# Kernel optimization log

Hardware: AMD Instinct MI355X
Metric: run time of the kernel (lower is better)

## Reference

```python
import jax, jax.numpy as jnp
import numpy as np

H_HEADS = 16
DECAY_C = 0.7408182206817179  # math.exp(-0.3)


def _gelu(x):
    return jax.nn.gelu(x, approximate=False)  # torch nn.GELU default = exact erf


def _mlp(x, W1, b1, W2, b2):
    return _gelu(x @ W1 + b1) @ W2 + b2


def setup_inputs():
    B, T, C = 4, 2048, 1024
    L = max(64, C // 8)      # lora_dim = 128
    E = int(C * 1.2)         # expanded_dim = 1228
    key = jax.random.key(0)
    ctr = [0]
    def rn(shape, s=0.02):
        ctr[0] += 1
        return jax.random.normal(jax.random.fold_in(key, ctr[0]), shape, jnp.float32) * s
    z = lambda *s: jnp.zeros(s, jnp.float32)
    inp = {
        "queries": rn((B, T, C), 1.0),
        "keys": rn((B, T, C), 1.0),
        "values": rn((B, T, C), 1.0),
        "attn_mask": jnp.ones((B, T), dtype=bool),
        "mu_r": rn((C,)), "mu_k": rn((C,)), "mu_v": rn((C,)),
        "mu_g": rn((C,)), "mu_a": rn((C,)), "mu_d": rn((C,)),
        "dA": rn((C, L)), "dB": rn((L, C)), "db": z(C),
        "aA": rn((C, L)), "aB": rn((L, C)), "ab": z(C),
        "gA": rn((C, L)), "gB": rn((L, C)),
        "rW1": rn((C, E)), "rb1": z(E), "rW2": rn((E, C)), "rb2": z(C),
        "kW1": rn((C, E)), "kb1": z(E), "kW2": rn((E, C)), "kb2": z(C),
        "vW1": rn((C, E)), "vb1": z(E), "vW2": rn((E, C)), "vb2": z(C),
        "oW1": rn((C, E)), "ob1": z(E), "oW2": rn((E, C)), "ob2": z(C),
        "rem_mult": rn((C,), 0.05),
        "iclr_mix": jnp.full((C,), 0.7, jnp.float32),
        "bonus_mult": jnp.full((C,), 1.2, jnp.float32),
        "ln_g": jnp.ones((C,), jnp.float32), "ln_b": z(C),
    }
    return inp


def _forward(queries, mu_r, mu_k, mu_v, mu_g, mu_a, mu_d,
             dA, dB, db, aA, aB, ab, gA, gB,
             rW1, rb1, rW2, rb2, kW1, kb1, kW2, kb2,
             vW1, vb1, vW2, vb2, oW1, ob1, oW2, ob2,
             rem_mult, iclr_mix, bonus_mult, ln_g, ln_b):
    B, T, C = queries.shape
    H = H_HEADS
    N = C // H
    r = _mlp(queries + mu_r, rW1, rb1, rW2, rb2)
    k = _mlp(queries + mu_k, kW1, kb1, kW2, kb2)
    v = _mlp(queries + mu_v, vW1, vb1, vW2, vb2)
    gate = jax.nn.sigmoid(((queries + mu_g) @ gA) @ gB)
    iclr = jax.nn.sigmoid(((queries + mu_a) @ aA) @ ab + ((queries + mu_a) @ aA) @ aB) if False else jax.nn.sigmoid(((queries + mu_a) @ aA) @ aB + ab)
    decay = jnp.exp(-DECAY_C * jax.nn.sigmoid(jnp.tanh(((queries + mu_d) @ dA) @ dB + db)))
    removal_k = k * rem_mult
    replacement_k = k * (1.0 + (iclr - 1.0) * iclr_mix)  # lerp(ones, iclr, mix)
    rh = r.reshape(B, T, H, N)
    rkh = replacement_k.reshape(B, T, H, N)
    vh = v.reshape(B, T, H, N)
    dh = decay.reshape(B, T, H, N)
    ah = iclr.reshape(B, T, H, N)
    rmh = removal_k.reshape(B, T, H, N)
    kn = rmh / jnp.maximum(jnp.linalg.norm(rmh, axis=-1, keepdims=True), 1e-12)  # F.normalize
    # Sequential matrix-state recurrence. G_t = diag(d) - kn (a*kn)^T, so
    # G_t @ S = d[:,None]*S - kn[:,None] * ((a*kn) @ S)  -- rank-1, O(N^2)/step.
    xs = tuple(jnp.swapaxes(a, 0, 1) for a in (dh, ah, kn, rkh, vh, rh))  # [T,B,H,N]
    def step(wkv, x):
        d, a, knt, rk, vt, rt = x
        tmp = jnp.einsum('bhj,bhjk->bhk', a * knt, wkv)
        wkv = d[..., None] * wkv - knt[..., None] * tmp[:, :, None, :] \
              + vt[..., None] * rk[:, :, None, :]
        return wkv, jnp.einsum('bhij,bhj->bhi', wkv, rt)
    wkv0 = jnp.zeros((B, H, N, N), queries.dtype)
    _, out_t = jax.lax.scan(step, wkv0, xs)
    out = jnp.swapaxes(out_t, 0, 1)  # [B,T,H,N]
    bonus = (jnp.sum(rh * rkh, -1, keepdims=True) * 0.2) * vh * bonus_mult.reshape(1, 1, H, N)
    out = (out + bonus).reshape(B, T, C)
    mu = jnp.mean(out, -1, keepdims=True)
    var = jnp.mean((out - mu) ** 2, -1, keepdims=True)
    out = (out - mu) / jnp.sqrt(var + 1e-6) * ln_g + ln_b  # ln_x, eps=1e-6
    out = out * gate
    out = _mlp(out, oW1, ob1, oW2, ob2)  # W_output; dropout is identity in eval
    return out


def reference(queries, keys, values, attn_mask,
              mu_r, mu_k, mu_v, mu_g, mu_a, mu_d,
              dA, dB, db, aA, aB, ab, gA, gB,
              rW1, rb1, rW2, rb2, kW1, kb1, kW2, kb2,
              vW1, vb1, vW2, vb2, oW1, ob1, oW2, ob2,
              rem_mult, iclr_mix, bonus_mult, ln_g, ln_b):
    del keys, values, attn_mask  # accepted but unused by the module's forward
    return _forward(queries, mu_r, mu_k, mu_v, mu_g, mu_a, mu_d,
                    dA, dB, db, aA, aB, ab, gA, gB,
                    rW1, rb1, rW2, rb2, kW1, kb1, kW2, kb2,
                    vW1, vb1, vW2, vb2, oW1, ob1, oW2, ob2,
                    rem_mult, iclr_mix, bonus_mult, ln_g, ln_b)
```

## Files before the change

### kernel.cpp

```cpp
#include <hip/hip_runtime.h>
#include <hip/hip_bf16.h>
#include <math.h>


#define BB 4
#define TT 2048
#define CC 1024
#define HH 16
#define NN 64
#define LL 128
#define EE 1228
#define EPAD 1280
#define MM (BB*TT)
#define TCH 32
#define NSEG 4
#define WARMCH 2
#define DECAY_C_F 0.7408182206817179f

typedef __attribute__((ext_vector_type(8))) short s16x8;
typedef __attribute__((ext_vector_type(4))) float f32x4;

#define GLOAD_LDS16(gp, lp) \
    __builtin_amdgcn_global_load_lds((const __attribute__((address_space(1))) void*)(gp), \
                                     (__attribute__((address_space(3))) void*)(lp), 16, 0, 0)

__global__ __launch_bounds__(256) void fold_pass1_z(
    const float* __restrict__ mu0, const float* __restrict__ mu1, const float* __restrict__ mu2,
    const float* __restrict__ W0,  const float* __restrict__ W1_, const float* __restrict__ W2_,
    float* __restrict__ partial, int ldW, int E, int ldP, int pslice) {
    const float* mu = blockIdx.z == 0 ? mu0 : (blockIdx.z == 1 ? mu1 : mu2);
    const float* W  = blockIdx.z == 0 ? W0  : (blockIdx.z == 1 ? W1_ : W2_);
    partial += (size_t)blockIdx.z * pslice;
    const int l = threadIdx.x & 63;
    const int e = blockIdx.x * 64 + l;
    const int pg = threadIdx.x >> 6;
    const int c0 = blockIdx.y * 64;
    float s = 0.f;
    if (e < E)
        for (int c = c0 + pg; c < c0 + 64; c += 4) s += mu[c] * W[(size_t)c * ldW + e];
    __shared__ float red[4][64];
    red[pg][l] = s;
    __syncthreads();
    if (pg == 0 && e < E)
        partial[(size_t)blockIdx.y * ldP + e] = red[0][l] + red[1][l] + red[2][l] + red[3][l];
}

__global__ void fold_pass2_z(const float* __restrict__ partial,
                             const float* b0, const float* b1, const float* b2,
                             float* __restrict__ outv,
                             int P, int ldP, int pslice, int E, int Epad, int oslice) {
    const float* bias = blockIdx.z == 0 ? b0 : (blockIdx.z == 1 ? b1 : b2);
    partial += (size_t)blockIdx.z * pslice;
    outv    += (size_t)blockIdx.z * oslice;
    int e = blockIdx.x * blockDim.x + threadIdx.x;
    if (e >= Epad) return;
    float s = 0.f;
    if (e < E) {
        s = bias ? bias[e] : 0.f;
        for (int p = 0; p < P; ++p) s += partial[(size_t)p * ldP + e];
    }
    outv[e] = s;
}

__global__ void cast_f32_bf16(const float* __restrict__ in, __hip_bfloat16* __restrict__ out, int n4) {
    int i = blockIdx.x * blockDim.x + threadIdx.x;
    if (i >= n4) return;
    float4 v = ((const float4*)in)[i];
    __hip_bfloat16 o[4] = {__float2bfloat16(v.x), __float2bfloat16(v.y),
                           __float2bfloat16(v.z), __float2bfloat16(v.w)};
    *(ulong1*)&out[i * 4] = *(ulong1*)o;
}

__global__ void transpose_cast_z(const float* s0, const float* s1, const float* s2,
                                 __hip_bfloat16* __restrict__ outT, size_t dslice,
                                 int Rin, int Cin, int Rpad, int Cpad) {
    const float* in = blockIdx.z == 0 ? s0 : (blockIdx.z == 1 ? s1 : s2);
    outT += (size_t)blockIdx.z * dslice;
    __shared__ float t[32][33];
    const int r0 = blockIdx.x * 32, c0 = blockIdx.y * 32;
    const int tx = threadIdx.x, ty = threadIdx.y;
    #pragma unroll
    for (int j = 0; j < 4; ++j) {
        int r = r0 + ty + j * 8, c = c0 + tx;
        t[ty + j * 8][tx] = (r < Rin && c < Cin) ? in[(size_t)r * Cin + c] : 0.f;
    }
    __syncthreads();
    #pragma unroll
    for (int j = 0; j < 4; ++j) {
        int c = c0 + ty + j * 8, r = r0 + tx;
        if (c < Cpad && r < Rpad) outT[(size_t)c * Rpad + r] = __float2bfloat16(t[tx][ty + j * 8]);
    }
}

template<int ACT, int OBF, int PADZ>
__global__ __launch_bounds__(256) void gemm_mfma(const __hip_bfloat16* __restrict__ A,
                                                 const __hip_bfloat16* __restrict__ Bt,
                                                 const float* __restrict__ bias,
                                                 void* __restrict__ Cptr,
                                                 int M, int N, int K,
                                                 int ldA, int ldB, int ldC,
                                                 size_t zA, size_t zB, size_t zBias, size_t zC) {
    __shared__ __hip_bfloat16 As[128 * 32];
    __shared__ __hip_bfloat16 Bs[128 * 32];
    const int tid = threadIdx.x;
    const int wid = tid >> 6, lane = tid & 63;
    const int wm = wid >> 1, wn = wid & 1;
    const int bm = blockIdx.y * 128, bn = blockIdx.x * 128;
    A  += (size_t)blockIdx.z * zA;
    Bt += (size_t)blockIdx.z * zB;
    if (bias) bias += (size_t)blockIdx.z * zBias;
    const size_t zc = (size_t)blockIdx.z * zC;

    const __hip_bfloat16* srcA[2];
    const __hip_bfloat16* srcB[2];
    #pragma unroll
    for (int i = 0; i < 2; ++i) {
        int off = (wid * 2 + i) * 1024 + lane * 16;
        int r = off >> 6;
        int c = (off >> 4) & 3;
        int cs = c ^ ((r >> 1) & 3);
        srcA[i] = A  + (size_t)(bm + r) * ldA + cs * 8;
        srcB[i] = Bt + (size_t)(bn + r) * ldB + cs * 8;
    }

    f32x4 acc[4][4];
    #pragma unroll
    for (int i = 0; i < 4; ++i)
        #pragma unroll
        for (int j = 0; j < 4; ++j) acc[i][j] = (f32x4){0.f, 0.f, 0.f, 0.f};

    for (int k0 = 0; k0 < K; k0 += 32) {
        #pragma unroll
        for (int i = 0; i < 2; ++i) {
            GLOAD_LDS16(srcA[i] + k0, (char*)As + (wid * 2 + i) * 1024);
            GLOAD_LDS16(srcB[i] + k0, (char*)Bs + (wid * 2 + i) * 1024);
        }
        __syncthreads();
        s16x8 af[4], bfr[4];
        #pragma unroll
        for (int mi = 0; mi < 4; ++mi) {
            int r = wm * 64 + mi * 16 + (lane & 15);
            int c = (lane >> 4) ^ ((r >> 1) & 3);
            af[mi] = *(const s16x8*)((const char*)As + r * 64 + c * 16);
        }
        #pragma unroll
        for (int ni = 0; ni < 4; ++ni) {
            int r = wn * 64 + ni * 16 + (lane & 15);
            int c = (lane >> 4) ^ ((r >> 1) & 3);
            bfr[ni] = *(const s16x8*)((const char*)Bs + r * 64 + c * 16);
        }
        #pragma unroll
        for (int mi = 0; mi < 4; ++mi)
            #pragma unroll
            for (int ni = 0; ni < 4; ++ni)
                acc[mi][ni] = __builtin_amdgcn_mfma_f32_16x16x32_bf16(af[mi], bfr[ni], acc[mi][ni], 0, 0, 0);
        __syncthreads();
    }

    #pragma unroll
    for (int ni = 0; ni < 4; ++ni) {
        const int col = bn + wn * 64 + ni * 16 + (lane & 15);
        const bool valid = (col < N);
        const float bc = (valid && bias) ? bias[col] : 0.f;
        #pragma unroll
        for (int mi = 0; mi < 4; ++mi) {
            #pragma unroll
            for (int reg = 0; reg < 4; ++reg) {
                const int row = bm + wm * 64 + mi * 16 + (lane >> 4) * 4 + reg;
                float y = 0.f;
                if (valid) {
                    float x = acc[mi][ni][reg] + bc;
                    if (ACT == 1)      y = 0.5f * x * (1.0f + erff(x * 0.7071067811865475f));
                    else if (ACT == 2) y = 1.0f / (1.0f + expf(-x));
                    else if (ACT == 3) { float sg = 1.0f / (1.0f + expf(-tanhf(x))); y = expf(-DECAY_C_F * sg); }
                    else               y = x;
                }
                if (valid || PADZ) {
                    if (OBF) ((__hip_bfloat16*)Cptr)[zc + (size_t)row * ldC + col] = __float2bfloat16(y);
                    else     ((float*)Cptr)[zc + (size_t)row * ldC + col] = y;
                }
            }
        }
    }
}

#define P_T0(i,j)   pool[0     + (i)*68 + (j)]
#define P_WT(i,j)   pool[4352  + (i)*68 + (j)]
#define P_KP(i,j)   pool[6528  + (i)*68 + (j)]
#define P_P2t(i,j)  pool[6528  + (i)*36 + (j)]
#define P_NU(i,j)   pool[8704  + (i)*68 + (j)]
#define P_GRt(i,j)  pool[8704  + (i)*36 + (j)]
#define P_RKM(i,j)  pool[10880 + (i)*68 + (j)]
#define P_RRM(i,j)  pool[13056 + (i)*68 + (j)]
#define P_GM(i,j)   pool[15232 + (i)*68 + (j)]
#define P_KPT(i,j)  pool[19712 + (i)*36 + (j)]
#define P_NUT(i,j)  pool[22016 + (i)*36 + (j)]
#define P_DCT(i,j)  pool[26624 + (i)*36 + (j)]
#define P_AT(i,j)   pool[28928 + (i)*36 + (j)]
#define P_BM(i,j)   pool[30080 + (i)*36 + (j)]
#define P_SEG(i,j)  pool[31232 + (i)*64 + (j)]
#define LD4(expr)   (*(const float4*)&(expr))
#define FMA4(acc, s, v) { (acc).x = fmaf((s), (v).x, (acc).x); (acc).y = fmaf((s), (v).y, (acc).y); \
                          (acc).z = fmaf((s), (v).z, (acc).z); (acc).w = fmaf((s), (v).w, (acc).w); }

__global__ __launch_bounds__(512) void recurrence_chunked(
    const float* __restrict__ kbuf, const __hip_bfloat16* __restrict__ iclr,
    const __hip_bfloat16* __restrict__ dbuf, const float* __restrict__ vbuf,
    const float* __restrict__ rbuf,
    const float* __restrict__ rem_mult, const float* __restrict__ iclr_mix,
    const float* __restrict__ bonus_mult, float* __restrict__ outb) {
    __shared__ float pool[31488];
    const int bh = blockIdx.x & 63, seg = blockIdx.x >> 6;
    const int b = bh >> 4, h = bh & 15;
    const int tid = threadIdx.x, lane = tid & 63, wid = tid >> 6;
    const size_t gbase = ((size_t)b * TT) * CC + (size_t)h * NN;

    for (int i = tid; i < 4352; i += 512) pool[i] = 0.f;
    const int c0 = tid & 63;
    const float remc = rem_mult[h * NN + c0];
    const float mixc = iclr_mix[h * NN + c0];
    __syncthreads();

    const int cout0 = (seg == 0) ? 0 : (seg == 1) ? 18 : (seg == 2) ? 34 : 49;
    const int lenq  = (seg == 0) ? 18 : (seg == 1) ? 16 : 15;
    const int ce    = cout0 + lenq;
    const int cb    = (seg == 0) ? 0 : cout0 - WARMCH;

    for (int chk = cb; chk < ce; ++chk) {
        const bool emit = (chk >= cout0);
        const int tg0 = chk * TCH;
        #pragma unroll
        for (int i = 0; i < 4; ++i) {
            int idx = tid + 512 * i;
            int t = idx >> 6, c = idx & 63;
            size_t off = gbase + (size_t)(tg0 + t) * CC + c;
            float kx = kbuf[off];
            float ax = __bfloat162float(iclr[off]);
            float rk = kx * (1.f + (ax - 1.f) * mixc);
            P_WT(t, c) = ax;
            P_KP(t, c) = kx * remc;
            P_RKM(t, c) = rk;
            P_NU(t, c) = vbuf[off];
            if (emit) P_RRM(t, c) = rbuf[off];
            P_DCT(c, t) = __bfloat162float(dbuf[off]);
        }
        __syncthreads();
        #pragma unroll
        for (int rr = 0; rr < 4; ++rr) {
            int t = wid + rr * 8;
            float v = P_KP(t, lane);
            float ss = v * v;
            #pragma unroll
            for (int s = 32; s; s >>= 1) ss += __shfl_xor(ss, s);
            float kn = v / fmaxf(sqrtf(ss), 1e-12f);
            P_KP(t, lane) = kn;
            P_WT(t, lane) = P_WT(t, lane) * kn;
        }
        float lc[8];
        const int ccs = tid & 63, sgm = tid >> 6, t0s = (sgm & 3) * 8;
        if (tid < 256) {
            float pp_ = 1.f;
            #pragma unroll
            for (int j = 0; j < 8; ++j) { pp_ *= P_DCT(ccs, t0s + j); lc[j] = pp_; }
            P_SEG(sgm, ccs) = pp_;
        }
        __syncthreads();
        if (tid < 256) {
            float m = 1.f;
            for (int s = 0; s < sgm; ++s) m *= P_SEG(s, ccs);
            float dcprev = m;
            #pragma unroll
            for (int j = 0; j < 8; ++j) {
                int t = t0s + j;
                float dcur = m * lc[j];
                P_WT(t, ccs) *= dcprev;
                float inv = 1.f / dcur;
                float kap = P_KP(t, ccs) * inv; P_KP(t, ccs) = kap; P_KPT(ccs, t) = kap;
                float nu  = P_NU(t, ccs) * inv; P_NU(t, ccs) = nu;  P_NUT(ccs, t) = nu;
                P_DCT(ccs, t) = dcur;
                dcprev = dcur;
            }
        }
        __syncthreads();
        #pragma unroll
        for (int u = 0; u < 2; ++u) {
            const int at = wid * 2 + u;
            const int s = (at >> 2) * 8 + (lane >> 3), t = (at & 3) * 8 + (lane & 7);
            float acc = 0.f;
            #pragma unroll
            for (int kc = 0; kc < 16; ++kc) {
                float4 a = LD4(P_KP(s, kc * 4));
                float4 bb = LD4(P_WT(t, kc * 4));
                acc += a.x * bb.x + a.y * bb.y + a.z * bb.z + a.w * bb.w;
            }
            P_AT(s, t) = (s < t) ? acc : 0.f;
        }
        #pragma unroll
        for (int u = 0; u < 2; ++u) {
            const int bt = wid * 2 + u;
            const int t = (bt >> 2) * 8 + (lane >> 3), s = (bt & 3) * 8 + (lane & 7);
            float acc = 0.f;
            #pragma unroll
            for (int kc = 0; kc < 16; ++kc) {
                float4 a = LD4(P_WT(t, kc * 4));
                float4 bb = LD4(P_NU(s, kc * 4));
                acc += a.x * bb.x + a.y * bb.y + a.z * bb.z + a.w * bb.w;
            }
            P_BM(t, s) = (s < t) ? acc : 0.f;
        }
        {
            const int t = wid * 4 + (lane >> 4);
            const int q4 = (lane & 15) * 4;
            float4 acc = {0.f, 0.f, 0.f, 0.f};
            #pragma unroll
            for (int j4 = 0; j4 < 16; ++j4) {
                float4 w4 = LD4(P_WT(t, j4 * 4));
                float4 ta = LD4(P_T0(j4 * 4 + 0, q4));
                float4 tb = LD4(P_T0(j4 * 4 + 1, q4));
                float4 tc = LD4(P_T0(j4 * 4 + 2, q4));
                float4 td = LD4(P_T0(j4 * 4 + 3, q4));
                FMA4(acc, w4.x, ta); FMA4(acc, w4.y, tb);
                FMA4(acc, w4.z, tc); FMA4(acc, w4.w, td);
            }
            *(float4*)&P_GM(t, q4) = acc;
        }
        __syncthreads();
        {
            const int t = wid * 4 + (lane >> 4);
            const int q4 = (lane & 15) * 4;
            float4 acc = {0.f, 0.f, 0.f, 0.f};
            #pragma unroll
            for (int s4 = 0; s4 < 8; ++s4) {
                float4 bm4 = LD4(P_BM(t, s4 * 4));
                float4 ra = LD4(P_RKM(s4 * 4 + 0, q4));
                float4 rb = LD4(P_RKM(s4 * 4 + 1, q4));
                float4 rc = LD4(P_RKM(s4 * 4 + 2, q4));
                float4 rd = LD4(P_RKM(s4 * 4 + 3, q4));
                FMA4(acc, bm4.x, ra); FMA4(acc, bm4.y, rb);
                FMA4(acc, bm4.z, rc); FMA4(acc, bm4.w, rd);
            }
            float4 g = LD4(P_GM(t, q4));
            g.x += acc.x; g.y += acc.y; g.z += acc.z; g.w += acc.w;
            *(float4*)&P_GM(t, q4) = g;
        }
        __syncthreads();
        if (wid == 0) {
            float g[32];
            #pragma unroll
            for (int t = 0; t < 32; ++t) g[t] = P_GM(t, lane);
            #pragma unroll
            for (int s = 0; s < 31; ++s) {
                #pragma unroll
                for (int t = s + 1; t < 32; ++t) g[t] -= P_AT(s, t) * g[s];
            }
            #pragma unroll
            for (int t = 0; t < 32; ++t) P_GM(t, lane) = g[t];
        } else if (emit) {
            for (int tile = wid - 1; tile < 16; tile += 7) {
                int t = (tile >> 2) * 8 + (lane >> 3), s = (tile & 3) * 8 + (lane & 7);
                float acc = 0.f;
                #pragma unroll
                for (int kc = 0; kc < 16; ++kc) {
                    float4 a = LD4(P_RRM(t, kc * 4));
                    float4 bb = LD4(P_RKM(s, kc * 4));
                    acc += a.x * bb.x + a.y * bb.y + a.z * bb.z + a.w * bb.w;
                }
                P_P2t(t, s) = (s <= t) ? acc : 0.f;
            }
        }
        __syncthreads();
        if (emit) {
            for (int tile = wid; tile < 16; tile += 8) {
                int t = (tile >> 2) * 8 + (lane >> 3), s = (tile & 3) * 8 + (lane & 7);
                float acc = 0.f;
                #pragma unroll
                for (int kc = 0; kc < 16; ++kc) {
                    float4 a = LD4(P_RRM(t, kc * 4));
                    float4 bb = LD4(P_GM(s, kc * 4));
                    acc += a.x * bb.x + a.y * bb.y + a.z * bb.z + a.w * bb.w;
                }
                P_GRt(t, s) = (s <= t) ? acc : 0.f;
            }
            __syncthreads();
            for (int tile = wid; tile < 32; tile += 8) {
                int i = (tile >> 2) * 8 + (lane >> 3), t = (tile & 3) * 8 + (lane & 7);
                float a1 = 0.f, a2 = 0.f, a3 = 0.f;
                #pragma unroll
                for (int j4 = 0; j4 < 16; ++j4) {
                    float4 a = LD4(P_T0(i, j4 * 4));
                    float4 bb = LD4(P_RRM(t, j4 * 4));
                    a1 += a.x * bb.x + a.y * bb.y + a.z * bb.z + a.w * bb.w;
                }
                #pragma unroll
                for (int s4 = 0; s4 < 8; ++s4) {
                    float4 a = LD4(P_NUT(i, s4 * 4));
                    float4 bb = LD4(P_P2t(t, s4 * 4));
                    a2 += a.x * bb.x + a.y * bb.y + a.z * bb.z + a.w * bb.w;
                    float4 c = LD4(P_KPT(i, s4 * 4));
                    float4 d = LD4(P_GRt(t, s4 * 4));
                    a3 += c.x * d.x + c.y * d.y + c.z * d.z + c.w * d.w;
                }
                float diag = 0.2f * bonus_mult[h * NN + i] * P_NUT(i, t) * P_P2t(t, t);
                outb[gbase + (size_t)(tg0 + t) * CC + i] = P_DCT(i, t) * (a1 + a2 + diag - a3);
            }
            __syncthreads();
        }
        #pragma unroll
        for (int u = 0; u < 2; ++u) {
            const int m = wid * 2 + u;
            const int pr = (m & 7) * 8 + (lane >> 3);
            const int q4 = (m >> 3) * 32 + (lane & 7) * 4;
            float4 a1 = {0.f, 0.f, 0.f, 0.f}, a2 = {0.f, 0.f, 0.f, 0.f};
            #pragma unroll
            for (int s = 0; s < 32; ++s) {
                const float kp = P_KPT(pr, s);
                const float nu = P_NUT(pr, s);
                float4 g4 = LD4(P_GM(s, q4));
                float4 rk4 = LD4(P_RKM(s, q4));
                FMA4(a1, kp, g4);
                FMA4(a2, nu, rk4);
            }
            const float dc = P_DCT(pr, 31);
            float4 t0 = LD4(P_T0(pr, q4));
            t0.x = dc * (t0.x - a1.x + a2.x);
            t0.y = dc * (t0.y - a1.y + a2.y);
            t0.z = dc * (t0.z - a1.z + a2.z);
            t0.w = dc * (t0.w - a1.w + a2.w);
            *(float4*)&P_T0(pr, q4) = t0;
        }
        __syncthreads();
    }
}

__global__ __launch_bounds__(256) void ln_gate_kernel(const float* __restrict__ x,
                                                      const __hip_bfloat16* __restrict__ gate,
                                                      const float* __restrict__ g,
                                                      const float* __restrict__ bv,
                                                      __hip_bfloat16* __restrict__ y) {
    const int row = blockIdx.x;
    const float* xr = x + (size_t)row * CC;
    float v[4];
    float s = 0.f;
    #pragma unroll
    for (int j = 0; j < 4; ++j) { v[j] = xr[threadIdx.x + 256 * j]; s += v[j]; }
    __shared__ float red[4], red2[4];
    #pragma unroll
    for (int o = 32; o; o >>= 1) s += __shfl_xor(s, o);
    if ((threadIdx.x & 63) == 0) red[threadIdx.x >> 6] = s;
    __syncthreads();
    const float mean = (red[0] + red[1] + red[2] + red[3]) * (1.f / CC);
    float vs = 0.f;
    #pragma unroll
    for (int j = 0; j < 4; ++j) { float d = v[j] - mean; vs += d * d; }
    #pragma unroll
    for (int o = 32; o; o >>= 1) vs += __shfl_xor(vs, o);
    if ((threadIdx.x & 63) == 0) red2[threadIdx.x >> 6] = vs;
    __syncthreads();
    const float var = (red2[0] + red2[1] + red2[2] + red2[3]) * (1.f / CC);
    const float rstd = rsqrtf(var + 1e-6f);
    #pragma unroll
    for (int j = 0; j < 4; ++j) {
        const int cc = threadIdx.x + 256 * j;
        float o_ = (v[j] - mean) * rstd * g[cc] + bv[cc];
        float gt = __bfloat162float(gate[(size_t)row * CC + cc]);
        y[(size_t)row * CC + cc] = __float2bfloat16(o_ * gt);
    }
}

extern "C" void kernel_launch(void* const* d_in, const int* in_sizes, int n_in,
                              void* d_out, int out_size, void* d_ws, size_t ws_size,
                              hipStream_t stream) {
    const float* q        = (const float*)d_in[0];
    const float* mu_r     = (const float*)d_in[4];
    const float* mu_k     = (const float*)d_in[5];
    const float* mu_v     = (const float*)d_in[6];
    const float* mu_g     = (const float*)d_in[7];
    const float* mu_a     = (const float*)d_in[8];
    const float* mu_d     = (const float*)d_in[9];
    const float* dA       = (const float*)d_in[10];
    const float* dB       = (const float*)d_in[11];
    const float* db       = (const float*)d_in[12];
    const float* aA       = (const float*)d_in[13];
    const float* aB       = (const float*)d_in[14];
    const float* ab       = (const float*)d_in[15];
    const float* gA       = (const float*)d_in[16];
    const float* gB       = (const float*)d_in[17];
    const float* rW1      = (const float*)d_in[18];
    const float* rb1      = (const float*)d_in[19];
    const float* rW2      = (const float*)d_in[20];
    const float* rb2      = (const float*)d_in[21];
    const float* kW1      = (const float*)d_in[22];
    const float* kb1      = (const float*)d_in[23];
    const float* kW2      = (const float*)d_in[24];
    const float* kb2      = (const float*)d_in[25];
    const float* vW1      = (const float*)d_in[26];
    const float* vb1      = (const float*)d_in[27];
    const float* vW2      = (const float*)d_in[28];
    const float* vb2      = (const float*)d_in[29];
    const float* oW1      = (const float*)d_in[30];
    const float* ob1      = (const float*)d_in[31];
    const float* oW2      = (const float*)d_in[32];
    const float* ob2      = (const float*)d_in[33];
    const float* rem_mult = (const float*)d_in[34];
    const float* iclr_mix = (const float*)d_in[35];
    const float* bonus_mult = (const float*)d_in[36];
    const float* ln_g     = (const float*)d_in[37];
    const float* ln_b     = (const float*)d_in[38];
    float* out = (float*)d_out;

    char* p = (char*)d_ws;
    auto alloc = [&](size_t bytes) { char* r = p; p += (bytes + 255) & ~(size_t)255; return r; };
    float* fb_all  = (float*)alloc((size_t)3 * EPAD * 4);
    float* c2_all  = (float*)alloc((size_t)3 * CC * 4);
    float* lt_all  = (float*)alloc((size_t)3 * LL * 4);
    float* cb2_all = (float*)alloc((size_t)3 * CC * 4);
    __hip_bfloat16* qb      = (__hip_bfloat16*)alloc((size_t)MM * CC * 2);
    __hip_bfloat16* W1T_all = (__hip_bfloat16*)alloc((size_t)3 * EPAD * CC * 2);
    __hip_bfloat16* W2T_all = (__hip_bfloat16*)alloc((size_t)3 * CC * EPAD * 2);
    __hip_bfloat16* Hb      = (__hip_bfloat16*)alloc((size_t)MM * 2 * EPAD * 2);
    float*          rkv     = (float*)alloc((size_t)3 * MM * CC * 4);
    __hip_bfloat16* abuf    = (__hip_bfloat16*)alloc((size_t)MM * CC * 2);
    __hip_bfloat16* dbuf    = (__hip_bfloat16*)alloc((size_t)MM * CC * 2);
    __hip_bfloat16* gbuf    = (__hip_bfloat16*)alloc((size_t)MM * CC * 2);
    float* rbuf = rkv;
    float* kbuf = rkv + (size_t)MM * CC;
    float* vbuf = rkv + (size_t)2 * MM * CC;
    float*          pp      = rkv;
    __hip_bfloat16* AT_all  = (__hip_bfloat16*)((char*)rkv + (1 << 18));
    __hip_bfloat16* BT_all  = (__hip_bfloat16*)((char*)rkv + (1 << 18) + 786432);
    __hip_bfloat16* oW1T    = (__hip_bfloat16*)rkv;
    __hip_bfloat16* oW2T    = (__hip_bfloat16*)((char*)rkv + 4194304);
    __hip_bfloat16* tgad    = Hb;

    const dim3 blk(256);
    const dim3 tblk(32, 8);

    hipMemcpyAsync(cb2_all,          rb2, CC * 4, hipMemcpyDeviceToDevice, stream);
    hipMemcpyAsync(cb2_all + CC,     kb2, CC * 4, hipMemcpyDeviceToDevice, stream);
    hipMemcpyAsync(cb2_all + 2 * CC, vb2, CC * 4, hipMemcpyDeviceToDevice, stream);

    fold_pass1_z<<<dim3(20, 16, 3), blk, 0, stream>>>(mu_r, mu_k, mu_v, rW1, kW1, vW1,
                                                      pp, EE, EE, EPAD, 16 * EPAD);
    fold_pass2_z<<<dim3(5, 1, 3), blk, 0, stream>>>(pp, rb1, kb1, vb1, fb_all,
                                                    16, EPAD, 16 * EPAD, EE, EPAD, EPAD);
    fold_pass1_z<<<dim3(2, 16, 3), blk, 0, stream>>>(mu_g, mu_a, mu_d, gA, aA, dA,
                                                     pp, LL, LL, EPAD, 16 * EPAD);
    fold_pass2_z<<<dim3(1, 1, 3), dim3(128), 0, stream>>>(pp, nullptr, nullptr, nullptr, lt_all,
                                                          16, EPAD, 16 * EPAD, LL, LL, LL);
    fold_pass1_z<<<dim3(16, 2, 3), blk, 0, stream>>>(lt_all, lt_all + LL, lt_all + 2 * LL, gB, aB, dB,
                                                     pp, CC, CC, EPAD, 16 * EPAD);
    fold_pass2_z<<<dim3(4, 1, 3), blk, 0, stream>>>(pp, nullptr, ab, db, c2_all,
                                                    2, EPAD, 16 * EPAD, CC, CC, CC);

    transpose_cast_z<<<dim3(32, 40, 3), tblk, 0, stream>>>(rW1, kW1, vW1, W1T_all,
                                                           (size_t)EPAD * CC, CC, EE, CC, EPAD);
    transpose_cast_z<<<dim3(40, 32, 3), tblk, 0, stream>>>(rW2, kW2, vW2, W2T_all,
                                                           (size_t)CC * EPAD, EE, CC, EPAD, CC);
    transpose_cast_z<<<dim3(32, 4, 3), tblk, 0, stream>>>(gA, aA, dA, AT_all,
                                                          (size_t)LL * CC, CC, LL, CC, LL);
    transpose_cast_z<<<dim3(4, 32, 3), tblk, 0, stream>>>(gB, aB, dB, BT_all,
                                                          (size_t)CC * LL, LL, CC, LL, CC);

    cast_f32_bf16<<<dim3(MM * CC / 4 / 256), blk, 0, stream>>>(q, qb, MM * CC / 4);

    gemm_mfma<0,1,0><<<dim3(3, 64, 1), blk, 0, stream>>>(qb, AT_all, nullptr, tgad,
                                                         MM, 384, CC, CC, CC, 384, 0, 0, 0, 0);
    gemm_mfma<2,1,0><<<dim3(8, 64, 1), blk, 0, stream>>>(tgad,       BT_all,               c2_all,          gbuf,
                                                         MM, CC, LL, 384, LL, CC, 0, 0, 0, 0);
    gemm_mfma<2,1,0><<<dim3(8, 64, 1), blk, 0, stream>>>(tgad + LL,  BT_all + (size_t)CC * LL,  c2_all + CC,     abuf,
                                                         MM, CC, LL, 384, LL, CC, 0, 0, 0, 0);
    gemm_mfma<3,1,0><<<dim3(8, 64, 1), blk, 0, stream>>>(tgad + 2 * LL, BT_all + (size_t)2 * CC * LL, c2_all + 2 * CC, dbuf,
                                                         MM, CC, LL, 384, LL, CC, 0, 0, 0, 0);

    gemm_mfma<1,1,0><<<dim3(20, 64, 1), blk, 0, stream>>>(qb, W1T_all, fb_all, Hb,
                                                          MM, 2 * EPAD, CC, CC, CC, 2 * EPAD, 0, 0, 0, 0);
    gemm_mfma<0,0,0><<<dim3(8, 64, 2), blk, 0, stream>>>(Hb, W2T_all, cb2_all, rkv,
                                                         MM, CC, EPAD, 2 * EPAD, EPAD, CC,
                                                         EPAD, (size_t)CC * EPAD, CC, (size_t)MM * CC);
    gemm_mfma<1,1,0><<<dim3(10, 64, 1), blk, 0, stream>>>(qb, W1T_all + (size_t)2 * EPAD * CC, fb_all + 2 * EPAD, Hb,
                                                          MM, EPAD, CC, CC, CC, EPAD, 0, 0, 0, 0);
    gemm_mfma<0,0,0><<<dim3(8, 64, 1), blk, 0, stream>>>(Hb, W2T_all + (size_t)2 * CC * EPAD, cb2_all + 2 * CC, vbuf,
                                                         MM, CC, EPAD, EPAD, EPAD, CC, 0, 0, 0, 0);

    recurrence_chunked<<<dim3(BB * HH * NSEG), dim3(512), 0, stream>>>(
        kbuf, abuf, dbuf, vbuf, rbuf, rem_mult, iclr_mix, bonus_mult, out);

    transpose_cast_z<<<dim3(32, 40, 1), tblk, 0, stream>>>(oW1, oW1, oW1, oW1T,
                                                           0, CC, EE, CC, EPAD);
    transpose_cast_z<<<dim3(40, 32, 1), tblk, 0, stream>>>(oW2, oW2, oW2, oW2T,
                                                           0, EE, CC, EPAD, CC);

    ln_gate_kernel<<<dim3(MM), blk, 0, stream>>>(out, gbuf, ln_g, ln_b, qb);

    gemm_mfma<1,1,1><<<dim3(10, 64, 1), blk, 0, stream>>>(qb, oW1T, ob1, Hb,
                                                          MM, EE, CC, CC, CC, EPAD, 0, 0, 0, 0);
    gemm_mfma<0,0,0><<<dim3(8, 64, 1), blk, 0, stream>>>(Hb, oW2T, ob2, out,
                                                         MM, CC, EPAD, EPAD, EPAD, CC, 0, 0, 0, 0);
}
```

Before: 939.7 us.

## Double GEMM K-tile to 64 and batch r/k/v and LoRA GEMMs

The MFMA GEMM now stages a 64-wide K slice per iteration with an 8-way XOR swizzle, which halves the number of barrier pairs per K loop. The three r/k/v first-layer GEMMs are merged into one wide launch and the second-layer GEMMs into one z-batched launch. The three LoRA up-projections (gate, iclr, decay) also run as one z-batched launch, with the activation chosen per z slice. Shared memory per block doubles, which may lower occupancy, and the hidden buffer grows to hold all three expansions.

```diff
diff --git a/kernel.cpp b/kernel.cpp
--- a/kernel.cpp
+++ b/kernel.cpp
@@ -92,7 +92,7 @@
     }
 }
 
-template<int ACT, int OBF, int PADZ>
+template<int ACT, int ACTZ2, int OBF, int PADZ>
 __global__ __launch_bounds__(256) void gemm_mfma(const __hip_bfloat16* __restrict__ A,
                                                  const __hip_bfloat16* __restrict__ Bt,
                                                  const float* __restrict__ bias,
@@ -100,8 +100,8 @@
                                                  int M, int N, int K,
                                                  int ldA, int ldB, int ldC,
                                                  size_t zA, size_t zB, size_t zBias, size_t zC) {
-    __shared__ __hip_bfloat16 As[128 * 32];
-    __shared__ __hip_bfloat16 Bs[128 * 32];
+    __shared__ __hip_bfloat16 As[128 * 64];
+    __shared__ __hip_bfloat16 Bs[128 * 64];
     const int tid = threadIdx.x;
     const int wid = tid >> 6, lane = tid & 63;
     const int wm = wid >> 1, wn = wid & 1;
@@ -110,15 +110,16 @@
     Bt += (size_t)blockIdx.z * zB;
     if (bias) bias += (size_t)blockIdx.z * zBias;
     const size_t zc = (size_t)blockIdx.z * zC;
-
-    const __hip_bfloat16* srcA[2];
-    const __hip_bfloat16* srcB[2];
-    #pragma unroll
-    for (int i = 0; i < 2; ++i) {
-        int off = (wid * 2 + i) * 1024 + lane * 16;
-        int r = off >> 6;
-        int c = (off >> 4) & 3;
-        int cs = c ^ ((r >> 1) & 3);
+    const int act = (ACTZ2 >= 0 && blockIdx.z == 2) ? ACTZ2 : ACT;
+
+    const __hip_bfloat16* srcA[4];
+    const __hip_bfloat16* srcB[4];
+    #pragma unroll
+    for (int i = 0; i < 4; ++i) {
+        int off = (wid * 4 + i) * 1024 + lane * 16;
+        int r = off >> 7;
+        int c = (off >> 4) & 7;
+        int cs = c ^ (r & 7);
         srcA[i] = A  + (size_t)(bm + r) * ldA + cs * 8;
         srcB[i] = Bt + (size_t)(bn + r) * ldB + cs * 8;
     }
@@ -129,31 +130,36 @@
         #pragma unroll
         for (int j = 0; j < 4; ++j) acc[i][j] = (f32x4){0.f, 0.f, 0.f, 0.f};
 
-    for (int k0 = 0; k0 < K; k0 += 32) {
-        #pragma unroll
-        for (int i = 0; i < 2; ++i) {
-            GLOAD_LDS16(srcA[i] + k0, (char*)As + (wid * 2 + i) * 1024);
-            GLOAD_LDS16(srcB[i] + k0, (char*)Bs + (wid * 2 + i) * 1024);
-        }
-        __syncthreads();
-        s16x8 af[4], bfr[4];
-        #pragma unroll
-        for (int mi = 0; mi < 4; ++mi) {
-            int r = wm * 64 + mi * 16 + (lane & 15);
-            int c = (lane >> 4) ^ ((r >> 1) & 3);
-            af[mi] = *(const s16x8*)((const char*)As + r * 64 + c * 16);
-        }
-        #pragma unroll
-        for (int ni = 0; ni < 4; ++ni) {
-            int r = wn * 64 + ni * 16 + (lane & 15);
-            int c = (lane >> 4) ^ ((r >> 1) & 3);
-            bfr[ni] = *(const s16x8*)((const char*)Bs + r * 64 + c * 16);
-        }
-        #pragma unroll
-        for (int mi = 0; mi < 4; ++mi)
-            #pragma unroll
-            for (int ni = 0; ni < 4; ++ni)
-                acc[mi][ni] = __builtin_amdgcn_mfma_f32_16x16x32_bf16(af[mi], bfr[ni], acc[mi][ni], 0, 0, 0);
+    const int ra = wm * 64 + (lane & 15);
+    const int rb = wn * 64 + (lane & 15);
+
+    for (int k0 = 0; k0 < K; k0 += 64) {
+        #pragma unroll
+        for (int i = 0; i < 4; ++i) {
+            GLOAD_LDS16(srcA[i] + k0, (char*)As + (wid * 4 + i) * 1024);
+            GLOAD_LDS16(srcB[i] + k0, (char*)Bs + (wid * 4 + i) * 1024);
+        }
+        __syncthreads();
+        #pragma unroll
+        for (int h = 0; h < 2; ++h) {
+            s16x8 af[4], bfr[4];
+            const int kc = (lane >> 4) + h * 4;
+            #pragma unroll
+            for (int mi = 0; mi < 4; ++mi) {
+                int r = ra + mi * 16;
+                af[mi] = *(const s16x8*)((const char*)As + r * 128 + (kc ^ (r & 7)) * 16);
+            }
+            #pragma unroll
+            for (int ni = 0; ni < 4; ++ni) {
+                int r = rb + ni * 16;
+                bfr[ni] = *(const s16x8*)((const char*)Bs + r * 128 + (kc ^ (r & 7)) * 16);
+            }
+            #pragma unroll
+            for (int mi = 0; mi < 4; ++mi)
+                #pragma unroll
+                for (int ni = 0; ni < 4; ++ni)
+                    acc[mi][ni] = __builtin_amdgcn_mfma_f32_16x16x32_bf16(af[mi], bfr[ni], acc[mi][ni], 0, 0, 0);
+        }
         __syncthreads();
     }
 
@@ -170,9 +176,9 @@
                 float y = 0.f;
                 if (valid) {
                     float x = acc[mi][ni][reg] + bc;
-                    if (ACT == 1)      y = 0.5f * x * (1.0f + erff(x * 0.7071067811865475f));
-                    else if (ACT == 2) y = 1.0f / (1.0f + expf(-x));
-                    else if (ACT == 3) { float sg = 1.0f / (1.0f + expf(-tanhf(x))); y = expf(-DECAY_C_F * sg); }
+                    if (act == 1)      y = 0.5f * x * (1.0f + erff(x * 0.7071067811865475f));
+                    else if (act == 2) y = 1.0f / (1.0f + expf(-x));
+                    else if (act == 3) { float sg = 1.0f / (1.0f + expf(-tanhf(x))); y = expf(-DECAY_C_F * sg); }
                     else               y = x;
                 }
                 if (valid || PADZ) {
@@ -517,11 +523,12 @@
     __hip_bfloat16* qb      = (__hip_bfloat16*)alloc((size_t)MM * CC * 2);
     __hip_bfloat16* W1T_all = (__hip_bfloat16*)alloc((size_t)3 * EPAD * CC * 2);
     __hip_bfloat16* W2T_all = (__hip_bfloat16*)alloc((size_t)3 * CC * EPAD * 2);
-    __hip_bfloat16* Hb      = (__hip_bfloat16*)alloc((size_t)MM * 2 * EPAD * 2);
+    __hip_bfloat16* Hb      = (__hip_bfloat16*)alloc((size_t)MM * 3 * EPAD * 2);
     float*          rkv     = (float*)alloc((size_t)3 * MM * CC * 4);
-    __hip_bfloat16* abuf    = (__hip_bfloat16*)alloc((size_t)MM * CC * 2);
-    __hip_bfloat16* dbuf    = (__hip_bfloat16*)alloc((size_t)MM * CC * 2);
-    __hip_bfloat16* gbuf    = (__hip_bfloat16*)alloc((size_t)MM * CC * 2);
+    __hip_bfloat16* gadbuf  = (__hip_bfloat16*)alloc((size_t)3 * MM * CC * 2);
+    __hip_bfloat16* gbuf = gadbuf;
+    __hip_bfloat16* abuf = gadbuf + (size_t)MM * CC;
+    __hip_bfloat16* dbuf = gadbuf + (size_t)2 * MM * CC;
     float* rbuf = rkv;
     float* kbuf = rkv + (size_t)MM * CC;
     float* vbuf = rkv + (size_t)2 * MM * CC;
@@ -563,24 +570,17 @@
 
     cast_f32_bf16<<<dim3(MM * CC / 4 / 256), blk, 0, stream>>>(q, qb, MM * CC / 4);
 
-    gemm_mfma<0,1,0><<<dim3(3, 64, 1), blk, 0, stream>>>(qb, AT_all, nullptr, tgad,
-                                                         MM, 384, CC, CC, CC, 384, 0, 0, 0, 0);
-    gemm_mfma<2,1,0><<<dim3(8, 64, 1), blk, 0, stream>>>(tgad,       BT_all,               c2_all,          gbuf,
-                                                         MM, CC, LL, 384, LL, CC, 0, 0, 0, 0);
-    gemm_mfma<2,1,0><<<dim3(8, 64, 1), blk, 0, stream>>>(tgad + LL,  BT_all + (size_t)CC * LL,  c2_all + CC,     abuf,
-                                                         MM, CC, LL, 384, LL, CC, 0, 0, 0, 0);
-    gemm_mfma<3,1,0><<<dim3(8, 64, 1), blk, 0, stream>>>(tgad + 2 * LL, BT_all + (size_t)2 * CC * LL, c2_all + 2 * CC, dbuf,
-                                                         MM, CC, LL, 384, LL, CC, 0, 0, 0, 0);
-
-    gemm_mfma<1,1,0><<<dim3(20, 64, 1), blk, 0, stream>>>(qb, W1T_all, fb_all, Hb,
-                                                          MM, 2 * EPAD, CC, CC, CC, 2 * EPAD, 0, 0, 0, 0);
-    gemm_mfma<0,0,0><<<dim3(8, 64, 2), blk, 0, stream>>>(Hb, W2T_all, cb2_all, rkv,
-                                                         MM, CC, EPAD, 2 * EPAD, EPAD, CC,
-                                                         EPAD, (size_t)CC * EPAD, CC, (size_t)MM * CC);
-    gemm_mfma<1,1,0><<<dim3(10, 64, 1), blk, 0, stream>>>(qb, W1T_all + (size_t)2 * EPAD * CC, fb_all + 2 * EPAD, Hb,
-                                                          MM, EPAD, CC, CC, CC, EPAD, 0, 0, 0, 0);
-    gemm_mfma<0,0,0><<<dim3(8, 64, 1), blk, 0, stream>>>(Hb, W2T_all + (size_t)2 * CC * EPAD, cb2_all + 2 * CC, vbuf,
-                                                         MM, CC, EPAD, EPAD, EPAD, CC, 0, 0, 0, 0);
+    gemm_mfma<0,-1,1,0><<<dim3(3, 64, 1), blk, 0, stream>>>(qb, AT_all, nullptr, tgad,
+                                                            MM, 384, CC, CC, CC, 384, 0, 0, 0, 0);
+    gemm_mfma<2,3,1,0><<<dim3(8, 64, 3), blk, 0, stream>>>(tgad, BT_all, c2_all, gadbuf,
+                                                           MM, CC, LL, 384, LL, CC,
+                                                           LL, (size_t)CC * LL, CC, (size_t)MM * CC);
+
+    gemm_mfma<1,-1,1,0><<<dim3(30, 64, 1), blk, 0, stream>>>(qb, W1T_all, fb_all, Hb,
+                                                             MM, 3 * EPAD, CC, CC, CC, 3 * EPAD, 0, 0, 0, 0);
+    gemm_mfma<0,-1,0,0><<<dim3(8, 64, 3), blk, 0, stream>>>(Hb, W2T_all, cb2_all, rkv,
+                                                            MM, CC, EPAD, 3 * EPAD, EPAD, CC,
+                                                            EPAD, (size_t)CC * EPAD, CC, (size_t)MM * CC);
 
     recurrence_chunked<<<dim3(BB * HH * NSEG), dim3(512), 0, stream>>>(
         kbuf, abuf, dbuf, vbuf, rbuf, rem_mult, iclr_mix, bonus_mult, out);
@@ -592,8 +592,8 @@
 
     ln_gate_kernel<<<dim3(MM), blk, 0, stream>>>(out, gbuf, ln_g, ln_b, qb);
 
-    gemm_mfma<1,1,1><<<dim3(10, 64, 1), blk, 0, stream>>>(qb, oW1T, ob1, Hb,
-                                                          MM, EE, CC, CC, CC, EPAD, 0, 0, 0, 0);
-    gemm_mfma<0,0,0><<<dim3(8, 64, 1), blk, 0, stream>>>(Hb, oW2T, ob2, out,
-                                                         MM, CC, EPAD, EPAD, EPAD, CC, 0, 0, 0, 0);
-}
+    gemm_mfma<1,-1,1,1><<<dim3(10, 64, 1), blk, 0, stream>>>(qb, oW1T, ob1, Hb,
+                                                             MM, EE, CC, CC, CC, EPAD, 0, 0, 0, 0);
+    gemm_mfma<0,-1,0,0><<<dim3(8, 64, 1), blk, 0, stream>>>(Hb, oW2T, ob2, out,
+                                                            MM, CC, EPAD, EPAD, EPAD, CC, 0, 0, 0, 0);
+}
```

Result: faster. 909.7 us (-3.2%).
